# Performance work log

Measured on AMD Instinct MI355X. Metric: run time of the kernel, lower is better.

## Reference

```python
import jax, jax.numpy as jnp
import numpy as np

B, SQ, SK, D, H = 4, 2048, 2048, 1024, 16
HD = D // H
SCALE = HD ** -0.5


def setup_inputs() -> dict:
    key = jax.random.key(0)
    ks = jax.random.split(key, 11)
    s = 0.02
    return {
        "query": jax.random.normal(ks[0], (B, SQ, D), jnp.float32),
        "key": jax.random.normal(ks[1], (B, SK, D), jnp.float32),
        "value": jax.random.normal(ks[2], (B, SK, D), jnp.float32),
        "Wq": jax.random.normal(ks[3], (D, D), jnp.float32) * s,
        "bq": jnp.zeros((D,), jnp.float32),
        "Wk": jax.random.normal(ks[4], (D, D), jnp.float32) * s,
        "bk": jnp.zeros((D,), jnp.float32),
        "Wv": jax.random.normal(ks[5], (D, D), jnp.float32) * s,
        "bv": jnp.zeros((D,), jnp.float32),
        "Wo": jax.random.normal(ks[6], (D, D), jnp.float32) * s,
        "bo": jnp.zeros((D,), jnp.float32),
    }


def reference(query, key, value, Wq, bq, Wk, bk, Wv, bv, Wo, bo):
    # Linear projections (torch nn.Linear: x @ W.T + b)
    Q = query @ Wq.T + bq          # (B, SQ, D)
    K = key @ Wk.T + bk            # (B, SK, D)
    V = value @ Wv.T + bv          # (B, SK, D)
    # split heads -> (B, H, S, HD)
    Q = Q.reshape(B, SQ, H, HD).transpose(0, 2, 1, 3)
    K = K.reshape(B, SK, H, HD).transpose(0, 2, 1, 3)
    V = V.reshape(B, SK, H, HD).transpose(0, 2, 1, 3)
    scores = jnp.einsum('bhqd,bhkd->bhqk', Q, K) * SCALE
    attn = jax.nn.softmax(scores, axis=-1)     # (B, H, SQ, SK); dropout=0 (eval)
    attended = jnp.einsum('bhqk,bhkd->bhqd', attn, V)
    attended = attended.mean(axis=1)           # head-average -> (B, SQ, HD)
    attended = jnp.tile(attended, (1, 1, H))   # repeat to (B, SQ, D)
    output = attended @ Wo.T + bo
    avg_attention = attn.mean(axis=1)          # (B, SQ, SK)
    return (output, avg_attention)
```

## Files before the change

### kernel.cpp

```cpp
#include <hip/hip_runtime.h>
#include <hip/hip_bf16.h>
#include <math.h>

#define BB 4
#define SQL 2048
#define SKL 2048
#define DM 1024
#define NH 16
#define HDIM 64
#define FSCALE 0.125f

typedef __attribute__((ext_vector_type(8))) short bf16x8;
typedef __attribute__((ext_vector_type(4))) float f32x4;
typedef __attribute__((ext_vector_type(16))) float f32x16;

__device__ __forceinline__ unsigned short f2bf(float f) {
    union { __hip_bfloat16 h; unsigned short u; } c;
    c.h = __float2bfloat16(f);
    return c.u;
}

__device__ __forceinline__ unsigned packbf(float lo, float hi) {
    return (unsigned)f2bf(lo) | ((unsigned)f2bf(hi) << 16);
}

__device__ __forceinline__ bf16x8 cvt8(const float4& a, const float4& b) {
    bf16x8 r;
    r[0] = (short)f2bf(a.x); r[1] = (short)f2bf(a.y);
    r[2] = (short)f2bf(a.z); r[3] = (short)f2bf(a.w);
    r[4] = (short)f2bf(b.x); r[5] = (short)f2bf(b.y);
    r[6] = (short)f2bf(b.z); r[7] = (short)f2bf(b.w);
    return r;
}

__device__ __forceinline__ void gload16(const void* g, void* l) {
    __builtin_amdgcn_global_load_lds(
        (const __attribute__((address_space(1))) unsigned int*)g,
        (__attribute__((address_space(3))) unsigned int*)l, 16, 0, 0);
}

#define VMCNT0() asm volatile("s_waitcnt vmcnt(0)" ::: "memory")

__global__ __launch_bounds__(256)
void wo_eff_kernel(const float* __restrict__ Wo, float* __restrict__ We) {
    int i = blockIdx.x * 256 + threadIdx.x;
    if (i < DM * HDIM) {
        int n = i >> 6, d = i & 63;
        float s = 0.f;
#pragma unroll
        for (int h = 0; h < NH; ++h) s += Wo[(size_t)n * DM + h * HDIM + d];
        We[i] = s;
    }
}

__global__ __launch_bounds__(256)
void proj_bf16(const float* __restrict__ X, const float* __restrict__ W,
               const float* __restrict__ bias, unsigned short* __restrict__ Y,
               float scale)
{
    __shared__ __align__(16) unsigned short As[128 * 32];
    __shared__ __align__(16) unsigned short Bs[128 * 32];
    const int tid = threadIdx.x;
    const int lane = tid & 63, wid = tid >> 6;
    const int g = lane >> 4, lm = lane & 15;
    const int wr = wid >> 1, wc = wid & 1;
    const int m0 = blockIdx.x * 128, n0 = blockIdx.y * 128;

    int rA[2], cA[2], offA[2];
#pragma unroll
    for (int i = 0; i < 2; ++i) {
        int q = tid + i * 256;
        rA[i] = q >> 2; cA[i] = q & 3;
        offA[i] = rA[i] * 32 + ((cA[i] ^ (rA[i] & 3)) << 3);
    }
    float4 xa[2][2], wa[2][2], xb[2][2], wb[2][2];
#pragma unroll
    for (int i = 0; i < 2; ++i) {
        const float* xp = &X[(size_t)(m0 + rA[i]) * DM + cA[i] * 8];
        const float* wp = &W[(size_t)(n0 + rA[i]) * DM + cA[i] * 8];
        xa[i][0] = *(const float4*)xp; xa[i][1] = *(const float4*)(xp + 4);
        wa[i][0] = *(const float4*)wp; wa[i][1] = *(const float4*)(wp + 4);
    }
    const f32x4 fz = {0.f, 0.f, 0.f, 0.f};
    f32x4 acc[4][4];
#pragma unroll
    for (int i = 0; i < 4; ++i)
#pragma unroll
        for (int j = 0; j < 4; ++j) acc[i][j] = fz;

    for (int t = 0; t < 32; ++t) {
        __syncthreads();
#pragma unroll
        for (int i = 0; i < 2; ++i) {
            *(bf16x8*)&As[offA[i]] = cvt8(xa[i][0], xa[i][1]);
            *(bf16x8*)&Bs[offA[i]] = cvt8(wa[i][0], wa[i][1]);
        }
        if (t < 31) {
            int k0 = (t + 1) * 32;
#pragma unroll
            for (int i = 0; i < 2; ++i) {
                const float* xp = &X[(size_t)(m0 + rA[i]) * DM + k0 + cA[i] * 8];
                const float* wp = &W[(size_t)(n0 + rA[i]) * DM + k0 + cA[i] * 8];
                xb[i][0] = *(const float4*)xp; xb[i][1] = *(const float4*)(xp + 4);
                wb[i][0] = *(const float4*)wp; wb[i][1] = *(const float4*)(wp + 4);
            }
        }
        __syncthreads();
        bf16x8 a[4], b[4];
#pragma unroll
        for (int f = 0; f < 4; ++f) {
            int ra = wr * 64 + f * 16 + lm;
            a[f] = *(const bf16x8*)&As[ra * 32 + (((g) ^ (ra & 3)) << 3)];
            int rb = wc * 64 + f * 16 + lm;
            b[f] = *(const bf16x8*)&Bs[rb * 32 + (((g) ^ (rb & 3)) << 3)];
        }
#pragma unroll
        for (int fm = 0; fm < 4; ++fm)
#pragma unroll
            for (int fn = 0; fn < 4; ++fn)
                acc[fm][fn] = __builtin_amdgcn_mfma_f32_16x16x32_bf16(
                    a[fm], b[fn], acc[fm][fn], 0, 0, 0);
        if (t < 31) {
#pragma unroll
            for (int i = 0; i < 2; ++i) {
                xa[i][0] = xb[i][0]; xa[i][1] = xb[i][1];
                wa[i][0] = wb[i][0]; wa[i][1] = wb[i][1];
            }
        }
    }
    float bn[4];
#pragma unroll
    for (int fn = 0; fn < 4; ++fn) bn[fn] = bias[n0 + wc * 64 + fn * 16 + lm];
#pragma unroll
    for (int fm = 0; fm < 4; ++fm)
#pragma unroll
        for (int i = 0; i < 4; ++i) {
            int m = m0 + wr * 64 + fm * 16 + 4 * g + i;
#pragma unroll
            for (int fn = 0; fn < 4; ++fn) {
                int n = n0 + wc * 64 + fn * 16 + lm;
                Y[(size_t)m * DM + n] = f2bf((acc[fm][fn][i] + bn[fn]) * scale);
            }
        }
}

__global__ __launch_bounds__(256)
void transpose_v(const unsigned short* __restrict__ V, unsigned short* __restrict__ Vt)
{
    __shared__ __align__(16) unsigned short Ts[64][80];
    const int tid = threadIdx.x;
    const int kv0 = blockIdx.x * 64, h = blockIdx.y, b = blockIdx.z;
#pragma unroll
    for (int i = 0; i < 2; ++i) {
        int q = tid + i * 256;
        int r = q >> 3, c = q & 7;
        *(uint4*)&Ts[r][c * 8] =
            *(const uint4*)&V[(size_t)(b * SKL + kv0 + r) * DM + h * HDIM + c * 8];
    }
    __syncthreads();
#pragma unroll
    for (int i = 0; i < 2; ++i) {
        int q = tid + i * 256;
        int d = q >> 3, kc = q & 7;
        union { unsigned short u16[8]; uint4 v; } tw;
#pragma unroll
        for (int e = 0; e < 8; ++e) tw.u16[e] = Ts[kc * 8 + e][d];
        *(uint4*)&Vt[((size_t)(b * NH + h) * HDIM + d) * SKL + kv0 + kc * 8] = tw.v;
    }
}

__global__ __launch_bounds__(256, 4)
void flash_mfma2(const unsigned short* __restrict__ Q,
                 const unsigned short* __restrict__ K,
                 const unsigned short* __restrict__ Vt,
                 float* __restrict__ mw, float* __restrict__ lw,
                 float* __restrict__ O)
{
    __shared__ __align__(16) unsigned short sK[2][64 * 64];
    __shared__ __align__(16) unsigned short sV[2][64 * 64];
    const int tid = threadIdx.x;
    const int lane = tid & 63, wid = tid >> 6;
    const int l31 = lane & 31, h8 = lane >> 5;
    const int q0 = blockIdx.x * 128, h = blockIdx.y, b = blockIdx.z;
    const int myq = q0 + wid * 32 + l31;

    bf16x8 qf[4];
    {
        const unsigned short* qp = &Q[(size_t)(b * SQL + myq) * DM + h * HDIM + h8 * 8];
#pragma unroll
        for (int c = 0; c < 4; ++c) qf[c] = *(const bf16x8*)(qp + c * 16);
    }

    int rr[2], cc[2];
#pragma unroll
    for (int i = 0; i < 2; ++i) {
        int s = tid + i * 256;
        rr[i] = s >> 3;
        cc[i] = ((s & 7) ^ (rr[i] & 7)) * 8;
    }
    const unsigned short* Kbase = &K[((size_t)b * SKL) * DM + h * HDIM];
    const unsigned short* Vbase = &Vt[((size_t)(b * NH + h) * HDIM) * SKL];

#pragma unroll
    for (int i = 0; i < 2; ++i) {
        gload16(Kbase + (size_t)rr[i] * DM + cc[i], &sK[0][(wid * 64 + i * 256) * 8]);
        gload16(Vbase + (size_t)rr[i] * SKL + cc[i], &sV[0][(wid * 64 + i * 256) * 8]);
    }
    VMCNT0();
    __syncthreads();

    const f32x16 z16 = {0.f};
    f32x16 o0 = z16, o1 = z16;
    float m_run = -INFINITY, l_run = 0.f;
    int cur = 0;

    for (int kt = 0; kt < SKL / 64; ++kt) {
        if (kt + 1 < SKL / 64) {
            int k0 = (kt + 1) * 64;
#pragma unroll
            for (int i = 0; i < 2; ++i) {
                gload16(Kbase + (size_t)(k0 + rr[i]) * DM + cc[i],
                        &sK[cur ^ 1][(wid * 64 + i * 256) * 8]);
                gload16(Vbase + (size_t)rr[i] * SKL + k0 + cc[i],
                        &sV[cur ^ 1][(wid * 64 + i * 256) * 8]);
            }
        }
        f32x16 c0 = z16, c1 = z16;
#pragma unroll
        for (int c = 0; c < 4; ++c) {
            int cg = 2 * c + h8;
            bf16x8 a0 = *(const bf16x8*)&sK[cur][l31 * 64 + ((cg ^ (l31 & 7)) << 3)];
            bf16x8 a1 = *(const bf16x8*)&sK[cur][(32 + l31) * 64 + ((cg ^ (l31 & 7)) << 3)];
            c0 = __builtin_amdgcn_mfma_f32_32x32x16_bf16(a0, qf[c], c0, 0, 0, 0);
            c1 = __builtin_amdgcn_mfma_f32_32x32x16_bf16(a1, qf[c], c1, 0, 0, 0);
        }
        float mx = c0[0];
#pragma unroll
        for (int r = 1; r < 16; ++r) mx = fmaxf(mx, c0[r]);
#pragma unroll
        for (int r = 0; r < 16; ++r) mx = fmaxf(mx, c1[r]);
        mx = fmaxf(mx, __shfl_xor(mx, 32));
        float mnew = fmaxf(m_run, mx);
        float fs = __expf(m_run - mnew);
        float ps = 0.f;
#pragma unroll
        for (int r = 0; r < 16; ++r) { c0[r] = __expf(c0[r] - mnew); ps += c0[r]; }
#pragma unroll
        for (int r = 0; r < 16; ++r) { c1[r] = __expf(c1[r] - mnew); ps += c1[r]; }
        ps += __shfl_xor(ps, 32);
        l_run = l_run * fs + ps;
        m_run = mnew;
        o0 *= fs;
        o1 *= fs;
        bf16x8 ap[4];
#pragma unroll
        for (int ks = 0; ks < 4; ++ks) {
            const int base = (ks & 1) * 8;
            f32x16 ct = (ks & 2) ? c1 : c0;
            unsigned wA0 = packbf(ct[base + 0], ct[base + 1]);
            unsigned wA1 = packbf(ct[base + 2], ct[base + 3]);
            unsigned wB0 = packbf(ct[base + 4], ct[base + 5]);
            unsigned wB1 = packbf(ct[base + 6], ct[base + 7]);
            asm volatile("v_permlane32_swap_b32 %0, %1" : "+v"(wA0), "+v"(wB0));
            asm volatile("v_permlane32_swap_b32 %0, %1" : "+v"(wA1), "+v"(wB1));
            union { unsigned u[4]; bf16x8 v; } pu;
            pu.u[0] = wA0; pu.u[1] = wA1; pu.u[2] = wB0; pu.u[3] = wB1;
            ap[ks] = pu.v;
        }
#pragma unroll
        for (int ks = 0; ks < 4; ++ks) {
            int cg = 2 * ks + h8;
            bf16x8 v0 = *(const bf16x8*)&sV[cur][l31 * 64 + ((cg ^ (l31 & 7)) << 3)];
            bf16x8 v1 = *(const bf16x8*)&sV[cur][(32 + l31) * 64 + ((cg ^ (l31 & 7)) << 3)];
            o0 = __builtin_amdgcn_mfma_f32_32x32x16_bf16(v0, ap[ks], o0, 0, 0, 0);
            o1 = __builtin_amdgcn_mfma_f32_32x32x16_bf16(v1, ap[ks], o1, 0, 0, 0);
        }
        VMCNT0();
        __syncthreads();
        cur ^= 1;
    }

    size_t mlidx = (size_t)(b * NH + h) * SQL + myq;
    if (h8 == 0) { mw[mlidx] = m_run; lw[mlidx] = l_run; }
    const float inv = 1.0f / (l_run * (float)NH);
    float* Op = &O[((size_t)(b * NH + h) * SQL + myq) * HDIM];
#pragma unroll
    for (int i2 = 0; i2 < 4; ++i2) {
        float4 w0, w1;
        w0.x = o0[4 * i2 + 0] * inv; w0.y = o0[4 * i2 + 1] * inv;
        w0.z = o0[4 * i2 + 2] * inv; w0.w = o0[4 * i2 + 3] * inv;
        w1.x = o1[4 * i2 + 0] * inv; w1.y = o1[4 * i2 + 1] * inv;
        w1.z = o1[4 * i2 + 2] * inv; w1.w = o1[4 * i2 + 3] * inv;
        int d = 8 * i2 + 4 * h8;
        *(float4*)(Op + d) = w0;
        *(float4*)(Op + d + 32) = w1;
    }
}

__global__ __launch_bounds__(256)
void am_reduce(const float* __restrict__ O, float* __restrict__ am)
{
    int i = blockIdx.x * 256 + threadIdx.x;
    int bq = i >> 4, c = i & 15;
    int b = bq >> 11, q = bq & 2047;
    const float* base = O + ((size_t)b * NH * SQL + q) * HDIM + c * 4;
    float4 s = {0.f, 0.f, 0.f, 0.f};
    for (int h = 0; h < NH; ++h) {
        float4 v = *(const float4*)(base + (size_t)h * SQL * HDIM);
        s.x += v.x; s.y += v.y; s.z += v.z; s.w += v.w;
    }
    *(float4*)(am + (size_t)bq * HDIM + c * 4) = s;
}

__global__ __launch_bounds__(256)
void avg_mfma(const unsigned short* __restrict__ Q, const unsigned short* __restrict__ K,
              const float* __restrict__ mw, const float* __restrict__ lw,
              float* __restrict__ avg)
{
    __shared__ __align__(16) unsigned short sQ[2][64 * 64];
    __shared__ __align__(16) unsigned short sK[2][64 * 64];
    __shared__ float mS[NH][64];
    __shared__ float ilS[NH][64];
    const int tid = threadIdx.x;
    const int lane = tid & 63, wid = tid >> 6;
    const int g = lane >> 4, lm = lane & 15;
    const int k0 = blockIdx.x * 64, q0 = blockIdx.y * 64, b = blockIdx.z;

    for (int i = tid; i < NH * 64; i += 256) {
        int hh = i >> 6, qq = i & 63;
        mS[hh][qq] = mw[(size_t)(b * NH + hh) * SQL + q0 + qq];
        ilS[hh][qq] = 1.0f / (lw[(size_t)(b * NH + hh) * SQL + q0 + qq] * (float)NH);
    }
    int rs[2], cs[2];
#pragma unroll
    for (int i = 0; i < 2; ++i) { int q = tid + i * 256; rs[i] = q >> 3; cs[i] = (q & 7) ^ (rs[i] & 7); }

    const unsigned short* Qbase = &Q[(size_t)(b * SQL + q0) * DM];
    const unsigned short* Kbase = &K[(size_t)(b * SKL + k0) * DM];
#pragma unroll
    for (int i = 0; i < 2; ++i) {
        gload16(Qbase + (size_t)rs[i] * DM + cs[i] * 8, &sQ[0][(tid + i * 256) * 8]);
        gload16(Kbase + (size_t)rs[i] * DM + cs[i] * 8, &sK[0][(tid + i * 256) * 8]);
    }
    VMCNT0();
    __syncthreads();

    const f32x4 fz = {0.f, 0.f, 0.f, 0.f};
    f32x4 acc[4];
#pragma unroll
    for (int nf = 0; nf < 4; ++nf) acc[nf] = fz;
    int cur = 0;
    for (int hh = 0; hh < NH; ++hh) {
        if (hh + 1 < NH) {
#pragma unroll
            for (int i = 0; i < 2; ++i) {
                gload16(Qbase + (size_t)rs[i] * DM + (hh + 1) * HDIM + cs[i] * 8,
                        &sQ[cur ^ 1][(tid + i * 256) * 8]);
                gload16(Kbase + (size_t)rs[i] * DM + (hh + 1) * HDIM + cs[i] * 8,
                        &sK[cur ^ 1][(tid + i * 256) * 8]);
            }
        }
        f32x4 s[4];
#pragma unroll
        for (int nf = 0; nf < 4; ++nf) s[nf] = fz;
#pragma unroll
        for (int kk = 0; kk < 2; ++kk) {
            int ra = wid * 16 + lm;
            bf16x8 a = *(const bf16x8*)&sQ[cur][ra * 64 + (((kk * 4 + g) ^ (ra & 7)) << 3)];
#pragma unroll
            for (int nf = 0; nf < 4; ++nf) {
                int r = nf * 16 + lm;
                bf16x8 kv = *(const bf16x8*)&sK[cur][r * 64 + (((kk * 4 + g) ^ (r & 7)) << 3)];
                s[nf] = __builtin_amdgcn_mfma_f32_16x16x32_bf16(a, kv, s[nf], 0, 0, 0);
            }
        }
#pragma unroll
        for (int i = 0; i < 4; ++i) {
            int ql = wid * 16 + 4 * g + i;
            float mv = mS[hh][ql], il = ilS[hh][ql];
#pragma unroll
            for (int nf = 0; nf < 4; ++nf)
                acc[nf][i] += __expf(s[nf][i] - mv) * il;
        }
        VMCNT0();
        __syncthreads();
        cur ^= 1;
    }
#pragma unroll
    for (int nf = 0; nf < 4; ++nf)
#pragma unroll
        for (int i = 0; i < 4; ++i)
            avg[(size_t)(b * SQL + q0 + wid * 16 + 4 * g + i) * SKL + k0 + nf * 16 + lm] =
                acc[nf][i];
}

__global__ __launch_bounds__(256)
void out_gemm(const float* __restrict__ amp, const float* __restrict__ We,
              const float* __restrict__ bo, float* __restrict__ out)
{
    __shared__ float As[64][68];
    __shared__ float Bs[64][68];
    const int m0 = blockIdx.x << 6, n0 = blockIdx.y << 6;
    const int tid = threadIdx.x;
    const int tx = tid & 15, ty = tid >> 4;
    const int lrow = tid >> 4, ldc = (tid & 15) << 2;
#pragma unroll
    for (int rr = 0; rr < 4; ++rr) {
        int r = (rr << 4) + lrow;
        float4 a = *reinterpret_cast<const float4*>(&amp[(size_t)(m0 + r) * HDIM + ldc]);
        float4 w = *reinterpret_cast<const float4*>(&We[(size_t)(n0 + r) * HDIM + ldc]);
        As[ldc + 0][r] = a.x; As[ldc + 1][r] = a.y; As[ldc + 2][r] = a.z; As[ldc + 3][r] = a.w;
        Bs[ldc + 0][r] = w.x; Bs[ldc + 1][r] = w.y; Bs[ldc + 2][r] = w.z; Bs[ldc + 3][r] = w.w;
    }
    __syncthreads();
    float acc[4][4] = {};
    for (int d = 0; d < 64; ++d) {
        float4 av = *reinterpret_cast<const float4*>(&As[d][ty << 2]);
        float4 bv = *reinterpret_cast<const float4*>(&Bs[d][tx << 2]);
        float aa[4] = {av.x, av.y, av.z, av.w};
        float bb[4] = {bv.x, bv.y, bv.z, bv.w};
#pragma unroll
        for (int i = 0; i < 4; ++i)
#pragma unroll
            for (int j = 0; j < 4; ++j)
                acc[i][j] = fmaf(aa[i], bb[j], acc[i][j]);
    }
    float4 bv = *reinterpret_cast<const float4*>(&bo[n0 + (tx << 2)]);
    float bb4[4] = {bv.x, bv.y, bv.z, bv.w};
#pragma unroll
    for (int i = 0; i < 4; ++i) {
        int m = m0 + (ty << 2) + i;
        float4 o = make_float4(acc[i][0] + bb4[0], acc[i][1] + bb4[1],
                               acc[i][2] + bb4[2], acc[i][3] + bb4[3]);
        *reinterpret_cast<float4*>(&out[(size_t)m * DM + n0 + (tx << 2)]) = o;
    }
}

extern "C" void kernel_launch(void* const* d_in, const int* in_sizes, int n_in,
                              void* d_out, int out_size, void* d_ws, size_t ws_size,
                              hipStream_t stream)
{
    const float* query = (const float*)d_in[0];
    const float* key   = (const float*)d_in[1];
    const float* value = (const float*)d_in[2];
    const float* Wq = (const float*)d_in[3];
    const float* bq = (const float*)d_in[4];
    const float* Wk = (const float*)d_in[5];
    const float* bk = (const float*)d_in[6];
    const float* Wv = (const float*)d_in[7];
    const float* bv = (const float*)d_in[8];
    const float* Wo = (const float*)d_in[9];
    const float* bo = (const float*)d_in[10];

    float* out0 = (float*)d_out;
    float* out_avg = out0 + (size_t)BB * SQL * DM;

    const size_t nQ = (size_t)BB * SQL * DM;
    const size_t nML = (size_t)BB * NH * SQL;
    const size_t nAM = (size_t)BB * SQL * HDIM;
    unsigned short* Qb = (unsigned short*)d_ws;
    unsigned short* Kb = Qb + nQ;
    unsigned short* Vb = Kb + nQ;
    unsigned short* Vt = Vb + nQ;
    float* Ob  = (float*)(Vt + nQ);
    float* mw  = Ob + (size_t)BB * NH * SQL * HDIM;
    float* lw  = mw + nML;
    float* amb = lw + nML;
    float* We  = amb + nAM;

    dim3 blk(256);
    wo_eff_kernel<<<dim3((DM * HDIM + 255) / 256), blk, 0, stream>>>(Wo, We);

    dim3 gp(64, 8);
    proj_bf16<<<gp, blk, 0, stream>>>(query, Wq, bq, Qb, FSCALE);
    proj_bf16<<<gp, blk, 0, stream>>>(key,   Wk, bk, Kb, 1.0f);
    proj_bf16<<<gp, blk, 0, stream>>>(value, Wv, bv, Vb, 1.0f);

    transpose_v<<<dim3(32, 16, 4), blk, 0, stream>>>(Vb, Vt);
    flash_mfma2<<<dim3(SQL / 128, NH, BB), blk, 0, stream>>>(Qb, Kb, Vt, mw, lw, Ob);
    am_reduce<<<dim3(512), blk, 0, stream>>>(Ob, amb);
    avg_mfma<<<dim3(32, 32, 4), blk, 0, stream>>>(Qb, Kb, mw, lw, out_avg);
    out_gemm<<<dim3(128, 16), blk, 0, stream>>>(amb, We, bo, out0);
}
```

Baseline: 352.9 us.

## Use base-2 softmax with lazy rescaling, fused log-sum stats, larger avg tiles

Folds log2(e) into the Q projection scale so both the flash kernel and the attention-average kernel use the hardware exp2 directly. The flash kernel skips rescaling unless the running max grows by more than 8, and emits one combined statistic, m + log2(16*l), instead of separate m and l. The avg-attention kernel then needs only a subtraction and an exp2 per element, and it moves to 128x128 tiles with 512 threads so each loaded K fragment is reused across two Q fragments. Packed bf16 conversion now uses a single v_cvt_pk_bf16_f32 instruction. The lazy rescale threshold allows exponentials up to 2^8 before rescaling, which relies on fp32 headroom.

```diff
diff --git a/kernel.cpp b/kernel.cpp
--- a/kernel.cpp
+++ b/kernel.cpp
@@ -8,11 +8,14 @@
 #define DM 1024
 #define NH 16
 #define HDIM 64
-#define FSCALE 0.125f
+#define QSCALE 0.18033688011112042f
 
 typedef __attribute__((ext_vector_type(8))) short bf16x8;
 typedef __attribute__((ext_vector_type(4))) float f32x4;
 typedef __attribute__((ext_vector_type(16))) float f32x16;
+
+__device__ __forceinline__ float exp2fast(float x) { return __builtin_amdgcn_exp2f(x); }
+__device__ __forceinline__ float log2fast(float x) { return __builtin_amdgcn_logf(x); }
 
 __device__ __forceinline__ unsigned short f2bf(float f) {
     union { __hip_bfloat16 h; unsigned short u; } c;
@@ -20,8 +23,10 @@
     return c.u;
 }
 
-__device__ __forceinline__ unsigned packbf(float lo, float hi) {
-    return (unsigned)f2bf(lo) | ((unsigned)f2bf(hi) << 16);
+__device__ __forceinline__ unsigned cvtpk(float lo, float hi) {
+    unsigned r;
+    asm("v_cvt_pk_bf16_f32 %0, %1, %2" : "=v"(r) : "v"(lo), "v"(hi));
+    return r;
 }
 
 __device__ __forceinline__ bf16x8 cvt8(const float4& a, const float4& b) {
@@ -173,8 +178,7 @@
 void flash_mfma2(const unsigned short* __restrict__ Q,
                  const unsigned short* __restrict__ K,
                  const unsigned short* __restrict__ Vt,
-                 float* __restrict__ mw, float* __restrict__ lw,
-                 float* __restrict__ O)
+                 float* __restrict__ uw, float* __restrict__ O)
 {
     __shared__ __align__(16) unsigned short sK[2][64 * 64];
     __shared__ __align__(16) unsigned short sV[2][64 * 64];
@@ -240,27 +244,30 @@
 #pragma unroll
         for (int r = 0; r < 16; ++r) mx = fmaxf(mx, c1[r]);
         mx = fmaxf(mx, __shfl_xor(mx, 32));
-        float mnew = fmaxf(m_run, mx);
-        float fs = __expf(m_run - mnew);
+        if (!__all(mx <= m_run + 8.0f)) {
+            float mnew = fmaxf(m_run, mx);
+            float fs = exp2fast(m_run - mnew);
+            l_run *= fs;
+            o0 *= fs;
+            o1 *= fs;
+            m_run = mnew;
+        }
         float ps = 0.f;
 #pragma unroll
-        for (int r = 0; r < 16; ++r) { c0[r] = __expf(c0[r] - mnew); ps += c0[r]; }
-#pragma unroll
-        for (int r = 0; r < 16; ++r) { c1[r] = __expf(c1[r] - mnew); ps += c1[r]; }
+        for (int r = 0; r < 16; ++r) { c0[r] = exp2fast(c0[r] - m_run); ps += c0[r]; }
+#pragma unroll
+        for (int r = 0; r < 16; ++r) { c1[r] = exp2fast(c1[r] - m_run); ps += c1[r]; }
         ps += __shfl_xor(ps, 32);
-        l_run = l_run * fs + ps;
-        m_run = mnew;
-        o0 *= fs;
-        o1 *= fs;
+        l_run += ps;
         bf16x8 ap[4];
 #pragma unroll
         for (int ks = 0; ks < 4; ++ks) {
             const int base = (ks & 1) * 8;
             f32x16 ct = (ks & 2) ? c1 : c0;
-            unsigned wA0 = packbf(ct[base + 0], ct[base + 1]);
-            unsigned wA1 = packbf(ct[base + 2], ct[base + 3]);
-            unsigned wB0 = packbf(ct[base + 4], ct[base + 5]);
-            unsigned wB1 = packbf(ct[base + 6], ct[base + 7]);
+            unsigned wA0 = cvtpk(ct[base + 0], ct[base + 1]);
+            unsigned wA1 = cvtpk(ct[base + 2], ct[base + 3]);
+            unsigned wB0 = cvtpk(ct[base + 4], ct[base + 5]);
+            unsigned wB1 = cvtpk(ct[base + 6], ct[base + 7]);
             asm volatile("v_permlane32_swap_b32 %0, %1" : "+v"(wA0), "+v"(wB0));
             asm volatile("v_permlane32_swap_b32 %0, %1" : "+v"(wA1), "+v"(wB1));
             union { unsigned u[4]; bf16x8 v; } pu;
@@ -281,7 +288,7 @@
     }
 
     size_t mlidx = (size_t)(b * NH + h) * SQL + myq;
-    if (h8 == 0) { mw[mlidx] = m_run; lw[mlidx] = l_run; }
+    if (h8 == 0) uw[mlidx] = m_run + log2fast(l_run * (float)NH);
     const float inv = 1.0f / (l_run * (float)NH);
     float* Op = &O[((size_t)(b * NH + h) * SQL + myq) * HDIM];
 #pragma unroll
@@ -312,86 +319,105 @@
     *(float4*)(am + (size_t)bq * HDIM + c * 4) = s;
 }
 
-__global__ __launch_bounds__(256)
-void avg_mfma(const unsigned short* __restrict__ Q, const unsigned short* __restrict__ K,
-              const float* __restrict__ mw, const float* __restrict__ lw,
-              float* __restrict__ avg)
-{
-    __shared__ __align__(16) unsigned short sQ[2][64 * 64];
-    __shared__ __align__(16) unsigned short sK[2][64 * 64];
-    __shared__ float mS[NH][64];
-    __shared__ float ilS[NH][64];
+__global__ __launch_bounds__(512)
+void avg_mfma2(const unsigned short* __restrict__ Q, const unsigned short* __restrict__ K,
+               const float* __restrict__ uw, float* __restrict__ avg)
+{
+    __shared__ __align__(16) unsigned short sQ[2][128 * 64];
+    __shared__ __align__(16) unsigned short sK[2][128 * 64];
+    __shared__ float uS[NH][128];
     const int tid = threadIdx.x;
     const int lane = tid & 63, wid = tid >> 6;
     const int g = lane >> 4, lm = lane & 15;
-    const int k0 = blockIdx.x * 64, q0 = blockIdx.y * 64, b = blockIdx.z;
-
-    for (int i = tid; i < NH * 64; i += 256) {
-        int hh = i >> 6, qq = i & 63;
-        mS[hh][qq] = mw[(size_t)(b * NH + hh) * SQL + q0 + qq];
-        ilS[hh][qq] = 1.0f / (lw[(size_t)(b * NH + hh) * SQL + q0 + qq] * (float)NH);
-    }
+    const int wq = wid >> 1, wk = wid & 1;
+    const int k0 = blockIdx.x * 128, q0 = blockIdx.y * 128, b = blockIdx.z;
+
+    for (int i = tid; i < NH * 128; i += 512) {
+        int hh = i >> 7, qq = i & 127;
+        uS[hh][qq] = uw[(size_t)(b * NH + hh) * SQL + q0 + qq];
+    }
+
     int rs[2], cs[2];
 #pragma unroll
-    for (int i = 0; i < 2; ++i) { int q = tid + i * 256; rs[i] = q >> 3; cs[i] = (q & 7) ^ (rs[i] & 7); }
-
+    for (int i = 0; i < 2; ++i) {
+        int s = tid + i * 512;
+        rs[i] = s >> 3;
+        cs[i] = (s & 7) ^ (rs[i] & 7);
+    }
     const unsigned short* Qbase = &Q[(size_t)(b * SQL + q0) * DM];
     const unsigned short* Kbase = &K[(size_t)(b * SKL + k0) * DM];
 #pragma unroll
     for (int i = 0; i < 2; ++i) {
-        gload16(Qbase + (size_t)rs[i] * DM + cs[i] * 8, &sQ[0][(tid + i * 256) * 8]);
-        gload16(Kbase + (size_t)rs[i] * DM + cs[i] * 8, &sK[0][(tid + i * 256) * 8]);
+        gload16(Qbase + (size_t)rs[i] * DM + cs[i] * 8, &sQ[0][(tid + i * 512) * 8]);
+        gload16(Kbase + (size_t)rs[i] * DM + cs[i] * 8, &sK[0][(tid + i * 512) * 8]);
     }
     VMCNT0();
     __syncthreads();
 
     const f32x4 fz = {0.f, 0.f, 0.f, 0.f};
-    f32x4 acc[4];
-#pragma unroll
-    for (int nf = 0; nf < 4; ++nf) acc[nf] = fz;
+    f32x4 acc[2][4];
+#pragma unroll
+    for (int mf = 0; mf < 2; ++mf)
+#pragma unroll
+        for (int nf = 0; nf < 4; ++nf) acc[mf][nf] = fz;
+
     int cur = 0;
     for (int hh = 0; hh < NH; ++hh) {
         if (hh + 1 < NH) {
 #pragma unroll
             for (int i = 0; i < 2; ++i) {
                 gload16(Qbase + (size_t)rs[i] * DM + (hh + 1) * HDIM + cs[i] * 8,
-                        &sQ[cur ^ 1][(tid + i * 256) * 8]);
+                        &sQ[cur ^ 1][(tid + i * 512) * 8]);
                 gload16(Kbase + (size_t)rs[i] * DM + (hh + 1) * HDIM + cs[i] * 8,
-                        &sK[cur ^ 1][(tid + i * 256) * 8]);
-            }
-        }
-        f32x4 s[4];
-#pragma unroll
-        for (int nf = 0; nf < 4; ++nf) s[nf] = fz;
+                        &sK[cur ^ 1][(tid + i * 512) * 8]);
+            }
+        }
+        f32x4 s[2][4];
+#pragma unroll
+        for (int mf = 0; mf < 2; ++mf)
+#pragma unroll
+            for (int nf = 0; nf < 4; ++nf) s[mf][nf] = fz;
 #pragma unroll
         for (int kk = 0; kk < 2; ++kk) {
-            int ra = wid * 16 + lm;
-            bf16x8 a = *(const bf16x8*)&sQ[cur][ra * 64 + (((kk * 4 + g) ^ (ra & 7)) << 3)];
+            bf16x8 a[2];
+#pragma unroll
+            for (int mf = 0; mf < 2; ++mf) {
+                int ra = wq * 32 + mf * 16 + lm;
+                a[mf] = *(const bf16x8*)&sQ[cur][ra * 64 + (((kk * 4 + g) ^ (ra & 7)) << 3)];
+            }
 #pragma unroll
             for (int nf = 0; nf < 4; ++nf) {
-                int r = nf * 16 + lm;
-                bf16x8 kv = *(const bf16x8*)&sK[cur][r * 64 + (((kk * 4 + g) ^ (r & 7)) << 3)];
-                s[nf] = __builtin_amdgcn_mfma_f32_16x16x32_bf16(a, kv, s[nf], 0, 0, 0);
-            }
-        }
-#pragma unroll
-        for (int i = 0; i < 4; ++i) {
-            int ql = wid * 16 + 4 * g + i;
-            float mv = mS[hh][ql], il = ilS[hh][ql];
-#pragma unroll
-            for (int nf = 0; nf < 4; ++nf)
-                acc[nf][i] += __expf(s[nf][i] - mv) * il;
-        }
+                int rb = wk * 64 + nf * 16 + lm;
+                bf16x8 kb = *(const bf16x8*)&sK[cur][rb * 64 + (((kk * 4 + g) ^ (rb & 7)) << 3)];
+#pragma unroll
+                for (int mf = 0; mf < 2; ++mf)
+                    s[mf][nf] = __builtin_amdgcn_mfma_f32_16x16x32_bf16(
+                        a[mf], kb, s[mf][nf], 0, 0, 0);
+            }
+        }
+#pragma unroll
+        for (int mf = 0; mf < 2; ++mf)
+#pragma unroll
+            for (int i4 = 0; i4 < 4; ++i4) {
+                float u = uS[hh][wq * 32 + mf * 16 + 4 * g + i4];
+#pragma unroll
+                for (int nf = 0; nf < 4; ++nf)
+                    acc[mf][nf][i4] += exp2fast(s[mf][nf][i4] - u);
+            }
         VMCNT0();
         __syncthreads();
         cur ^= 1;
     }
 #pragma unroll
-    for (int nf = 0; nf < 4; ++nf)
-#pragma unroll
-        for (int i = 0; i < 4; ++i)
-            avg[(size_t)(b * SQL + q0 + wid * 16 + 4 * g + i) * SKL + k0 + nf * 16 + lm] =
-                acc[nf][i];
+    for (int mf = 0; mf < 2; ++mf)
+#pragma unroll
+        for (int i4 = 0; i4 < 4; ++i4) {
+            int qrow = q0 + wq * 32 + mf * 16 + 4 * g + i4;
+#pragma unroll
+            for (int nf = 0; nf < 4; ++nf)
+                avg[(size_t)(b * SQL + qrow) * SKL + k0 + wk * 64 + nf * 16 + lm] =
+                    acc[mf][nf][i4];
+        }
 }
 
 __global__ __launch_bounds__(256)
@@ -463,22 +489,21 @@
     unsigned short* Vb = Kb + nQ;
     unsigned short* Vt = Vb + nQ;
     float* Ob  = (float*)(Vt + nQ);
-    float* mw  = Ob + (size_t)BB * NH * SQL * HDIM;
-    float* lw  = mw + nML;
-    float* amb = lw + nML;
+    float* uw  = Ob + (size_t)BB * NH * SQL * HDIM;
+    float* amb = uw + nML;
     float* We  = amb + nAM;
 
     dim3 blk(256);
     wo_eff_kernel<<<dim3((DM * HDIM + 255) / 256), blk, 0, stream>>>(Wo, We);
 
     dim3 gp(64, 8);
-    proj_bf16<<<gp, blk, 0, stream>>>(query, Wq, bq, Qb, FSCALE);
+    proj_bf16<<<gp, blk, 0, stream>>>(query, Wq, bq, Qb, QSCALE);
     proj_bf16<<<gp, blk, 0, stream>>>(key,   Wk, bk, Kb, 1.0f);
     proj_bf16<<<gp, blk, 0, stream>>>(value, Wv, bv, Vb, 1.0f);
 
     transpose_v<<<dim3(32, 16, 4), blk, 0, stream>>>(Vb, Vt);
-    flash_mfma2<<<dim3(SQL / 128, NH, BB), blk, 0, stream>>>(Qb, Kb, Vt, mw, lw, Ob);
+    flash_mfma2<<<dim3(SQL / 128, NH, BB), blk, 0, stream>>>(Qb, Kb, Vt, uw, Ob);
     am_reduce<<<dim3(512), blk, 0, stream>>>(Ob, amb);
-    avg_mfma<<<dim3(32, 32, 4), blk, 0, stream>>>(Qb, Kb, mw, lw, out_avg);
+    avg_mfma2<<<dim3(SKL / 128, SQL / 128, BB), dim3(512), 0, stream>>>(Qb, Kb, uw, out_avg);
     out_gemm<<<dim3(128, 16), blk, 0, stream>>>(amb, We, bo, out0);
 }
```

Result: faster. 313.7 us (-11.1%).
